# Kernel optimization log

Measured on AMD Instinct MI355X. Metric: run time of the kernel, lower is better.

## Reference

```python
import jax, jax.numpy as jnp
import numpy as np

N_NODES = 500_000
N_EDGES = 16_000_000


def setup_inputs() -> dict:
    key = jax.random.key(0)
    ks = jax.random.split(key, 8)
    x = jax.random.normal(ks[0], (N_NODES, 6), dtype=jnp.float32)
    edge_index = jax.random.randint(ks[1], (2, N_EDGES), 0, N_NODES, dtype=jnp.int64)
    conv_w = jax.random.normal(ks[2], (4, 6), dtype=jnp.float32) * 0.4
    conv_b = jax.random.normal(ks[3], (4,), dtype=jnp.float32) * 0.1
    fc1_w = jax.random.normal(ks[4], (64, 4), dtype=jnp.float32) * 0.5
    fc1_b = jax.random.normal(ks[5], (64,), dtype=jnp.float32) * 0.1
    fc3_w = jax.random.normal(ks[6], (10, 64), dtype=jnp.float32) * 0.125
    fc3_b = jax.random.normal(ks[7], (10,), dtype=jnp.float32) * 0.1
    return {"x": x, "edge_index": edge_index, "conv_w": conv_w, "conv_b": conv_b,
            "fc1_w": fc1_w, "fc1_b": fc1_b, "fc3_w": fc3_w, "fc3_b": fc3_b}


def reference(x, edge_index, conv_w, conv_b, fc1_w, fc1_b, fc3_w, fc3_b):
    n = x.shape[0]
    loop = jnp.arange(n, dtype=edge_index.dtype)
    # PyG GCNConv default: add self-loops, symmetric normalization
    row = jnp.concatenate([edge_index[0], loop])  # source
    col = jnp.concatenate([edge_index[1], loop])  # target (aggregation index)
    deg = jax.ops.segment_sum(jnp.ones_like(col, dtype=x.dtype), col, num_segments=n)
    dinv = jnp.where(deg > 0, deg ** -0.5, 0.0).astype(x.dtype)
    norm = dinv[row] * dinv[col]                  # [E+N]
    h = x @ conv_w.T                              # [N, 4]
    msg = h[row] * norm[:, None]                  # gather + scale
    agg = jax.ops.segment_sum(msg, col, num_segments=n) + conv_b  # scatter-add
    t = jnp.tanh(agg)
    # F.dropout treated as identity (deterministic eval reference)
    g = jnp.mean(t, axis=0, keepdims=True)        # global_mean_pool, batch=None -> [1, 4]
    hdn = jax.nn.relu(g @ fc1_w.T + fc1_b)
    out = hdn @ fc3_w.T + fc3_b                   # [1, output_size]
    return out
```

## Files before the change

### kernel.cpp

```cpp
#include <hip/hip_runtime.h>
#include <hip/hip_fp16.h>
#include <math.h>


constexpr int NP = 1024;
constexpr int SHIFT = 10;
constexpr unsigned MASK = 1023;
constexpr int NPART_MAX = 512;
constexpr int EPB = 8192;
constexpr int BINB = 512;
constexpr int BT = 512;

struct alignas(8) Half4 { __half2 a, b; };


__global__ __launch_bounds__(BINB) void k_bin(const int* __restrict__ row,
                                              const int* __restrict__ col, int E,
                                              int P, int cap, int* __restrict__ cursor,
                                              unsigned* __restrict__ binned) {
    __shared__ unsigned lbuf[EPB];
    __shared__ int lcount[NPART_MAX];
    __shared__ int lbase[NPART_MAX];
    __shared__ int gbase[NPART_MAX];
    __shared__ int lpos[NPART_MAX];
    __shared__ int sc[NPART_MAX];

    int t = threadIdx.x;
    int start = blockIdx.x * EPB;
    int end = min(start + EPB, E);
    bool full = (end - start) == EPB;

    lcount[t] = 0; lpos[t] = 0;
    __syncthreads();

    if (full) {
        const int4* c4 = (const int4*)(col + start);
#pragma unroll
        for (int i = 0; i < EPB / 4 / BINB; ++i) {
            int4 c = c4[t + i * BINB];
            atomicAdd(&lcount[c.x >> SHIFT], 1);
            atomicAdd(&lcount[c.y >> SHIFT], 1);
            atomicAdd(&lcount[c.z >> SHIFT], 1);
            atomicAdd(&lcount[c.w >> SHIFT], 1);
        }
    } else {
        for (int e = start + t; e < end; e += BINB)
            atomicAdd(&lcount[col[e] >> SHIFT], 1);
    }
    __syncthreads();

    sc[t] = lcount[t];
    __syncthreads();
    for (int off = 1; off < NPART_MAX; off <<= 1) {
        int v = (t >= off) ? sc[t - off] : 0;
        __syncthreads();
        sc[t] += v;
        __syncthreads();
    }
    lbase[t] = sc[t] - lcount[t];
    if (t < P) {
        int c = lcount[t];
        gbase[t] = (c > 0) ? atomicAdd(&cursor[t], c) : 0;
    }
    __syncthreads();

    if (full) {
        const int4* c4 = (const int4*)(col + start);
        const int4* r4 = (const int4*)(row + start);
#pragma unroll
        for (int i = 0; i < EPB / 4 / BINB; ++i) {
            int4 c = c4[t + i * BINB];
            int4 r = r4[t + i * BINB];
            int part, slot;
            part = c.x >> SHIFT; slot = atomicAdd(&lpos[part], 1);
            lbuf[lbase[part] + slot] = ((unsigned)r.x << SHIFT) | ((unsigned)c.x & MASK);
            part = c.y >> SHIFT; slot = atomicAdd(&lpos[part], 1);
            lbuf[lbase[part] + slot] = ((unsigned)r.y << SHIFT) | ((unsigned)c.y & MASK);
            part = c.z >> SHIFT; slot = atomicAdd(&lpos[part], 1);
            lbuf[lbase[part] + slot] = ((unsigned)r.z << SHIFT) | ((unsigned)c.z & MASK);
            part = c.w >> SHIFT; slot = atomicAdd(&lpos[part], 1);
            lbuf[lbase[part] + slot] = ((unsigned)r.w << SHIFT) | ((unsigned)c.w & MASK);
        }
    } else {
        for (int e = start + t; e < end; e += BINB) {
            int r = row[e], c = col[e];
            int part = c >> SHIFT;
            int slot = atomicAdd(&lpos[part], 1);
            lbuf[lbase[part] + slot] = ((unsigned)r << SHIFT) | ((unsigned)c & MASK);
        }
    }
    __syncthreads();

    int lane = t & 63;
    int wave = t >> 6;
    const int nwaves = BINB / 64;
    for (int part = wave; part < P; part += nwaves) {
        int cnt = lcount[part];
        if (cnt == 0) continue;
        int lb = lbase[part];
        int gb = gbase[part];
        unsigned* dst = binned + (size_t)part * cap;
        for (int j = lane; j < cnt; j += 64) {
            int slot = gb + j;
            if (slot < cap) dst[slot] = lbuf[lb + j];
        }
    }
}

__global__ __launch_bounds__(BT) void k_part_node(const unsigned* __restrict__ binned,
                                                  const int* __restrict__ cursor, int cap,
                                                  const float* __restrict__ x,
                                                  const float* __restrict__ conv_w, int n,
                                                  Half4* __restrict__ ph,
                                                  float* __restrict__ dinvg) {
    __shared__ int degs[NP];
    __shared__ float w[24];
    int part = blockIdx.x;
    int tid = threadIdx.x;
    if (tid < 24) w[tid] = conv_w[tid];
    for (int i = tid; i < NP; i += BT) degs[i] = 0;
    __syncthreads();
    int cnt = min(cursor[part], cap);
    const unsigned* bin = binned + (size_t)part * cap;
    const uint4* bin4 = (const uint4*)bin;
    int cnt4 = cnt >> 2;
    for (int i = tid; i < cnt4; i += BT) {
        uint4 v = bin4[i];
        atomicAdd(&degs[v.x & MASK], 1);
        atomicAdd(&degs[v.y & MASK], 1);
        atomicAdd(&degs[v.z & MASK], 1);
        atomicAdd(&degs[v.w & MASK], 1);
    }
    for (int e = (cnt4 << 2) + tid; e < cnt; e += BT)
        atomicAdd(&degs[bin[e] & MASK], 1);
    __syncthreads();
    int base = part * NP;
    for (int i = tid; i < NP; i += BT) {
        int node = base + i;
        if (node >= n) continue;
        float dinv = rsqrtf((float)(degs[i] + 1));
        const float* xr = x + (size_t)node * 6;
        float2 a = *(const float2*)xr;
        float2 b = *(const float2*)(xr + 2);
        float2 cc = *(const float2*)(xr + 4);
        float xv[6] = {a.x, a.y, b.x, b.y, cc.x, cc.y};
        float h0 = 0.f, h1 = 0.f, h2 = 0.f, h3 = 0.f;
#pragma unroll
        for (int j = 0; j < 6; ++j) {
            h0 += xv[j] * w[j];
            h1 += xv[j] * w[6 + j];
            h2 += xv[j] * w[12 + j];
            h3 += xv[j] * w[18 + j];
        }
        Half4 o;
        o.a = __floats2half2_rn(h0 * dinv, h1 * dinv);
        o.b = __floats2half2_rn(h2 * dinv, h3 * dinv);
        ph[node] = o;
        dinvg[node] = dinv;
    }
}

__global__ __launch_bounds__(BT) void k_acc(const unsigned* __restrict__ binned,
                                            const int* __restrict__ cursor, int cap,
                                            const Half4* __restrict__ ph,
                                            const float* __restrict__ dinvg,
                                            const float* __restrict__ conv_b, int n,
                                            float* __restrict__ gsum) {
    __shared__ float S[NP * 5];
    __shared__ float4 red[BT / 64];
    int part = blockIdx.x;
    int tid = threadIdx.x;
    for (int i = tid; i < NP * 5; i += BT) S[i] = 0.f;
    __syncthreads();
    int cnt = min(cursor[part], cap);
    const unsigned* bin = binned + (size_t)part * cap;
    const uint4* bin4 = (const uint4*)bin;
    int cnt4 = cnt >> 2;
    for (int i = tid; i < cnt4; i += BT) {
        uint4 v = bin4[i];
        Half4 h0 = ph[v.x >> SHIFT];
        Half4 h1 = ph[v.y >> SHIFT];
        Half4 h2 = ph[v.z >> SHIFT];
        Half4 h3 = ph[v.w >> SHIFT];
        float2 a, b; float* s;
        a = __half22float2(h0.a); b = __half22float2(h0.b); s = &S[(v.x & MASK) * 5];
        atomicAdd(s + 0, a.x); atomicAdd(s + 1, a.y); atomicAdd(s + 2, b.x); atomicAdd(s + 3, b.y);
        a = __half22float2(h1.a); b = __half22float2(h1.b); s = &S[(v.y & MASK) * 5];
        atomicAdd(s + 0, a.x); atomicAdd(s + 1, a.y); atomicAdd(s + 2, b.x); atomicAdd(s + 3, b.y);
        a = __half22float2(h2.a); b = __half22float2(h2.b); s = &S[(v.z & MASK) * 5];
        atomicAdd(s + 0, a.x); atomicAdd(s + 1, a.y); atomicAdd(s + 2, b.x); atomicAdd(s + 3, b.y);
        a = __half22float2(h3.a); b = __half22float2(h3.b); s = &S[(v.w & MASK) * 5];
        atomicAdd(s + 0, a.x); atomicAdd(s + 1, a.y); atomicAdd(s + 2, b.x); atomicAdd(s + 3, b.y);
    }
    for (int e = (cnt4 << 2) + tid; e < cnt; e += BT) {
        unsigned v = bin[e];
        Half4 h = ph[v >> SHIFT];
        float2 a = __half22float2(h.a), b = __half22float2(h.b);
        float* s = &S[(v & MASK) * 5];
        atomicAdd(s + 0, a.x); atomicAdd(s + 1, a.y); atomicAdd(s + 2, b.x); atomicAdd(s + 3, b.y);
    }
    __syncthreads();
    float b0 = conv_b[0], b1 = conv_b[1], b2 = conv_b[2], b3 = conv_b[3];
    float4 acc = {0.f, 0.f, 0.f, 0.f};
    int base = part * NP;
    for (int i = tid; i < NP; i += BT) {
        int node = base + i;
        if (node >= n) continue;
        float di = dinvg[node];
        Half4 hp = ph[node];
        float2 pa = __half22float2(hp.a), pb = __half22float2(hp.b);
        acc.x += tanhf(di * (S[i * 5 + 0] + pa.x) + b0);
        acc.y += tanhf(di * (S[i * 5 + 1] + pa.y) + b1);
        acc.z += tanhf(di * (S[i * 5 + 2] + pb.x) + b2);
        acc.w += tanhf(di * (S[i * 5 + 3] + pb.y) + b3);
    }
#pragma unroll
    for (int off = 32; off > 0; off >>= 1) {
        acc.x += __shfl_down(acc.x, off);
        acc.y += __shfl_down(acc.y, off);
        acc.z += __shfl_down(acc.z, off);
        acc.w += __shfl_down(acc.w, off);
    }
    int lane = tid & 63, wv = tid >> 6;
    if (lane == 0) red[wv] = acc;
    __syncthreads();
    if (tid == 0) {
        float4 tt = red[0];
        for (int k = 1; k < BT / 64; ++k) {
            tt.x += red[k].x; tt.y += red[k].y; tt.z += red[k].z; tt.w += red[k].w;
        }
        unsafeAtomicAdd(&gsum[0], tt.x);
        unsafeAtomicAdd(&gsum[1], tt.y);
        unsafeAtomicAdd(&gsum[2], tt.z);
        unsafeAtomicAdd(&gsum[3], tt.w);
    }
}

__global__ void k_head(const float* __restrict__ gsum,
                       const float* __restrict__ fc1w, const float* __restrict__ fc1b,
                       const float* __restrict__ fc3w, const float* __restrict__ fc3b,
                       float* __restrict__ out, int n) {
    __shared__ float hdn[64];
    int t = threadIdx.x;
    float g[4];
    float inv_n = 1.0f / (float)n;
#pragma unroll
    for (int j = 0; j < 4; ++j) g[j] = gsum[j] * inv_n;
    if (t < 64) {
        float a = fc1b[t];
#pragma unroll
        for (int j = 0; j < 4; ++j) a += g[j] * fc1w[t * 4 + j];
        hdn[t] = fmaxf(a, 0.f);
    }
    __syncthreads();
    if (t < 10) {
        float a = fc3b[t];
#pragma unroll
        for (int k = 0; k < 64; ++k) a += hdn[k] * fc3w[t * 64 + k];
        out[t] = a;
    }
}


__global__ void k_deg(const int* __restrict__ col, int n_edges, int* __restrict__ deg) {
    int t = blockIdx.x * blockDim.x + threadIdx.x;
    int base = t * 4;
    if (base + 4 <= n_edges) {
        int4 c = *(const int4*)(col + base);
        atomicAdd(&deg[c.x], 1); atomicAdd(&deg[c.y], 1);
        atomicAdd(&deg[c.z], 1); atomicAdd(&deg[c.w], 1);
    } else {
        for (int e = base; e < n_edges; ++e) atomicAdd(&deg[col[e]], 1);
    }
}

__global__ void k_node(const float* __restrict__ x, const float* __restrict__ conv_w,
                       const int* __restrict__ deg, float4* __restrict__ p, int n) {
    int i = blockIdx.x * blockDim.x + threadIdx.x;
    if (i >= n) return;
    const float* xr = x + (size_t)i * 6;
    float2 a = *(const float2*)xr;
    float2 b = *(const float2*)(xr + 2);
    float2 c = *(const float2*)(xr + 4);
    float xv[6] = {a.x, a.y, b.x, b.y, c.x, c.y};
    float dinv = rsqrtf((float)(deg[i] + 1));
    float h0 = 0.f, h1 = 0.f, h2 = 0.f, h3 = 0.f;
#pragma unroll
    for (int j = 0; j < 6; ++j) {
        h0 += xv[j] * conv_w[j];
        h1 += xv[j] * conv_w[6 + j];
        h2 += xv[j] * conv_w[12 + j];
        h3 += xv[j] * conv_w[18 + j];
    }
    float4 o; o.x = h0 * dinv; o.y = h1 * dinv; o.z = h2 * dinv; o.w = h3 * dinv;
    p[i] = o;
}

__global__ void k_scatter(const int* __restrict__ row, const int* __restrict__ col, int n_edges,
                          const float4* __restrict__ p, float* __restrict__ S) {
    int t = blockIdx.x * blockDim.x + threadIdx.x;
    int base = t * 2;
    if (base + 2 <= n_edges) {
        int2 r = *(const int2*)(row + base);
        int2 c = *(const int2*)(col + base);
        float4 p0 = p[r.x], p1 = p[r.y];
        float* s0 = S + 4 * c.x;
        unsafeAtomicAdd(s0 + 0, p0.x); unsafeAtomicAdd(s0 + 1, p0.y);
        unsafeAtomicAdd(s0 + 2, p0.z); unsafeAtomicAdd(s0 + 3, p0.w);
        float* s1 = S + 4 * c.y;
        unsafeAtomicAdd(s1 + 0, p1.x); unsafeAtomicAdd(s1 + 1, p1.y);
        unsafeAtomicAdd(s1 + 2, p1.z); unsafeAtomicAdd(s1 + 3, p1.w);
    } else {
        for (int e = base; e < n_edges; ++e) {
            int r = row[e], c = col[e];
            float4 pv = p[r];
            float* s = S + 4 * c;
            unsafeAtomicAdd(s + 0, pv.x); unsafeAtomicAdd(s + 1, pv.y);
            unsafeAtomicAdd(s + 2, pv.z); unsafeAtomicAdd(s + 3, pv.w);
        }
    }
}

__global__ void k_reduce(const float4* __restrict__ S4, const float4* __restrict__ p,
                         const int* __restrict__ deg, const float* __restrict__ conv_b,
                         int n, float* __restrict__ gsum) {
    int i = blockIdx.x * blockDim.x + threadIdx.x;
    float4 v = {0.f, 0.f, 0.f, 0.f};
    if (i < n) {
        float dinv = rsqrtf((float)(deg[i] + 1));
        float4 s = S4[i];
        float4 pp = p[i];
        v.x = tanhf(dinv * (s.x + pp.x) + conv_b[0]);
        v.y = tanhf(dinv * (s.y + pp.y) + conv_b[1]);
        v.z = tanhf(dinv * (s.z + pp.z) + conv_b[2]);
        v.w = tanhf(dinv * (s.w + pp.w) + conv_b[3]);
    }
#pragma unroll
    for (int off = 32; off > 0; off >>= 1) {
        v.x += __shfl_down(v.x, off);
        v.y += __shfl_down(v.y, off);
        v.z += __shfl_down(v.z, off);
        v.w += __shfl_down(v.w, off);
    }
    __shared__ float4 lds[4];
    int lane = threadIdx.x & 63, w = threadIdx.x >> 6;
    if (lane == 0) lds[w] = v;
    __syncthreads();
    if (threadIdx.x == 0) {
        float4 tt = lds[0];
        for (int k = 1; k < 4; ++k) {
            tt.x += lds[k].x; tt.y += lds[k].y; tt.z += lds[k].z; tt.w += lds[k].w;
        }
        unsafeAtomicAdd(&gsum[0], tt.x); unsafeAtomicAdd(&gsum[1], tt.y);
        unsafeAtomicAdd(&gsum[2], tt.z); unsafeAtomicAdd(&gsum[3], tt.w);
    }
}


extern "C" void kernel_launch(void* const* d_in, const int* in_sizes, int n_in,
                              void* d_out, int out_size, void* d_ws, size_t ws_size,
                              hipStream_t stream) {
    const float* x      = (const float*)d_in[0];
    const int*   ei     = (const int*)d_in[1];
    const float* conv_w = (const float*)d_in[2];
    const float* conv_b = (const float*)d_in[3];
    const float* fc1w   = (const float*)d_in[4];
    const float* fc1b   = (const float*)d_in[5];
    const float* fc3w   = (const float*)d_in[6];
    const float* fc3b   = (const float*)d_in[7];

    int n = in_sizes[0] / 6;
    int E = in_sizes[1] / 2;
    const int* row = ei;
    const int* col = ei + E;

    int P = (n + NP - 1) / NP;
    int avg = (E + P - 1) / P;
    int cap = ((avg + avg / 8 + 2048) + 15) & ~15;

    size_t off = 0;
    size_t cursor_off = off;          off += (size_t)P * sizeof(int);
    off = (off + 15) & ~(size_t)15;
    size_t gsum_off = off;            off += 4 * sizeof(float);
    size_t zero_end = off;
    off = (off + 15) & ~(size_t)15;
    size_t dinv_off = off;            off += (size_t)n * sizeof(float);
    off = (off + 15) & ~(size_t)15;
    size_t ph_off = off;              off += (size_t)n * sizeof(Half4);
    off = (off + 15) & ~(size_t)15;
    size_t bin_off = off;             off += (size_t)P * cap * sizeof(unsigned);
    size_t need = off;

    char* ws = (char*)d_ws;
    bool use_bin = (ws_size >= need) && (P <= NPART_MAX) && (n < (1 << 22));

    if (use_bin) {
        int* cursor = (int*)(ws + cursor_off);
        float* gsum = (float*)(ws + gsum_off);
        float* dinvg = (float*)(ws + dinv_off);
        Half4* ph = (Half4*)(ws + ph_off);
        unsigned* binned = (unsigned*)(ws + bin_off);

        hipMemsetAsync(d_ws, 0, zero_end, stream);
        int bin_blocks = (E + EPB - 1) / EPB;
        k_bin<<<bin_blocks, BINB, 0, stream>>>(row, col, E, P, cap, cursor, binned);
        k_part_node<<<P, BT, 0, stream>>>(binned, cursor, cap, x, conv_w, n, ph, dinvg);
        k_acc<<<P, BT, 0, stream>>>(binned, cursor, cap, ph, dinvg, conv_b, n, gsum);
        k_head<<<1, 64, 0, stream>>>(gsum, fc1w, fc1b, fc3w, fc3b, (float*)d_out, n);
    } else {
        size_t o = 0;
        int* deg = (int*)(ws + o);      o += (size_t)n * sizeof(int);
        o = (o + 15) & ~(size_t)15;
        float* S = (float*)(ws + o);    o += (size_t)n * 4 * sizeof(float);
        float* gsum = (float*)(ws + o);
        size_t zend = o + 4 * sizeof(float);
        o = (zend + 15) & ~(size_t)15;
        float4* p = (float4*)(ws + o);

        hipMemsetAsync(d_ws, 0, zend, stream);
        int t1 = (E + 3) / 4;
        k_deg<<<(t1 + 255) / 256, 256, 0, stream>>>(col, E, deg);
        k_node<<<(n + 255) / 256, 256, 0, stream>>>(x, conv_w, deg, p, n);
        int t3 = (E + 1) / 2;
        k_scatter<<<(t3 + 255) / 256, 256, 0, stream>>>(row, col, E, p, S);
        k_reduce<<<(n + 255) / 256, 256, 0, stream>>>((const float4*)S, p, deg, conv_b, n, gsum);
        k_head<<<1, 64, 0, stream>>>(gsum, fc1w, fc1b, fc3w, fc3b, (float*)d_out, n);
    }
}
```

Measured before the change: 624.5 us.

## Split per-partition accumulation across sub-blocks and move tanh reduction to separate kernel

The accumulation kernel now runs SUB blocks per partition. Each block accumulates its share of the binned edges in shared memory and writes a partial sum array to global memory. A new kernel adds up the partials for each node, applies tanh and reduces the result into the global sum. The change also unrolls the edge loop by two, switches to unsafeAtomicAdd on shared memory, and shrinks the bin capacity slack. The aim is more parallelism: P is about 489 blocks on a large GPU, so this doubles it. The cost is an extra kernel launch, extra global traffic for the partials, and a higher risk of bin overflow with the smaller capacity.

```diff
diff --git a/kernel.cpp b/kernel.cpp
--- a/kernel.cpp
+++ b/kernel.cpp
@@ -160,15 +160,23 @@
     }
 }
 
-__global__ __launch_bounds__(BT) void k_acc(const unsigned* __restrict__ binned,
-                                            const int* __restrict__ cursor, int cap,
-                                            const Half4* __restrict__ ph,
-                                            const float* __restrict__ dinvg,
-                                            const float* __restrict__ conv_b, int n,
-                                            float* __restrict__ gsum) {
+__device__ __forceinline__ void acc_edge(float* __restrict__ S, unsigned v,
+                                         const Half4& h) {
+    float2 a = __half22float2(h.a), b = __half22float2(h.b);
+    float* s = &S[(v & MASK) * 5];
+    unsafeAtomicAdd(s + 0, a.x);
+    unsafeAtomicAdd(s + 1, a.y);
+    unsafeAtomicAdd(s + 2, b.x);
+    unsafeAtomicAdd(s + 3, b.y);
+}
+
+__global__ __launch_bounds__(BT) void k_acc2(const unsigned* __restrict__ binned,
+                                             const int* __restrict__ cursor, int cap,
+                                             const Half4* __restrict__ ph, int SUB,
+                                             float4* __restrict__ Spart) {
     __shared__ float S[NP * 5];
-    __shared__ float4 red[BT / 64];
-    int part = blockIdx.x;
+    int part = blockIdx.x / SUB;
+    int sub = blockIdx.x - part * SUB;
     int tid = threadIdx.x;
     for (int i = tid; i < NP * 5; i += BT) S[i] = 0.f;
     __syncthreads();
@@ -176,43 +184,72 @@
     const unsigned* bin = binned + (size_t)part * cap;
     const uint4* bin4 = (const uint4*)bin;
     int cnt4 = cnt >> 2;
-    for (int i = tid; i < cnt4; i += BT) {
+    int chunk4 = (cnt4 + SUB - 1) / SUB;
+    int s4 = sub * chunk4;
+    int e4 = min(cnt4, s4 + chunk4);
+
+    int i = s4 + tid;
+    for (; i + BT < e4; i += 2 * BT) {
+        uint4 v0 = bin4[i];
+        uint4 v1 = bin4[i + BT];
+        Half4 h0 = ph[v0.x >> SHIFT];
+        Half4 h1 = ph[v0.y >> SHIFT];
+        Half4 h2 = ph[v0.z >> SHIFT];
+        Half4 h3 = ph[v0.w >> SHIFT];
+        Half4 h4 = ph[v1.x >> SHIFT];
+        Half4 h5 = ph[v1.y >> SHIFT];
+        Half4 h6 = ph[v1.z >> SHIFT];
+        Half4 h7 = ph[v1.w >> SHIFT];
+        acc_edge(S, v0.x, h0); acc_edge(S, v0.y, h1);
+        acc_edge(S, v0.z, h2); acc_edge(S, v0.w, h3);
+        acc_edge(S, v1.x, h4); acc_edge(S, v1.y, h5);
+        acc_edge(S, v1.z, h6); acc_edge(S, v1.w, h7);
+    }
+    for (; i < e4; i += BT) {
         uint4 v = bin4[i];
         Half4 h0 = ph[v.x >> SHIFT];
         Half4 h1 = ph[v.y >> SHIFT];
         Half4 h2 = ph[v.z >> SHIFT];
         Half4 h3 = ph[v.w >> SHIFT];
-        float2 a, b; float* s;
-        a = __half22float2(h0.a); b = __half22float2(h0.b); s = &S[(v.x & MASK) * 5];
-        atomicAdd(s + 0, a.x); atomicAdd(s + 1, a.y); atomicAdd(s + 2, b.x); atomicAdd(s + 3, b.y);
-        a = __half22float2(h1.a); b = __half22float2(h1.b); s = &S[(v.y & MASK) * 5];
-        atomicAdd(s + 0, a.x); atomicAdd(s + 1, a.y); atomicAdd(s + 2, b.x); atomicAdd(s + 3, b.y);
-        a = __half22float2(h2.a); b = __half22float2(h2.b); s = &S[(v.z & MASK) * 5];
-        atomicAdd(s + 0, a.x); atomicAdd(s + 1, a.y); atomicAdd(s + 2, b.x); atomicAdd(s + 3, b.y);
-        a = __half22float2(h3.a); b = __half22float2(h3.b); s = &S[(v.w & MASK) * 5];
-        atomicAdd(s + 0, a.x); atomicAdd(s + 1, a.y); atomicAdd(s + 2, b.x); atomicAdd(s + 3, b.y);
-    }
-    for (int e = (cnt4 << 2) + tid; e < cnt; e += BT) {
-        unsigned v = bin[e];
-        Half4 h = ph[v >> SHIFT];
-        float2 a = __half22float2(h.a), b = __half22float2(h.b);
-        float* s = &S[(v & MASK) * 5];
-        atomicAdd(s + 0, a.x); atomicAdd(s + 1, a.y); atomicAdd(s + 2, b.x); atomicAdd(s + 3, b.y);
-    }
-    __syncthreads();
-    float b0 = conv_b[0], b1 = conv_b[1], b2 = conv_b[2], b3 = conv_b[3];
+        acc_edge(S, v.x, h0); acc_edge(S, v.y, h1);
+        acc_edge(S, v.z, h2); acc_edge(S, v.w, h3);
+    }
+    if (sub == SUB - 1) {
+        for (int e = (cnt4 << 2) + tid; e < cnt; e += BT)
+            acc_edge(S, bin[e], ph[bin[e] >> SHIFT]);
+    }
+    __syncthreads();
+    float4* dst = Spart + (size_t)blockIdx.x * NP;
+    for (int k = tid; k < NP; k += BT) {
+        float4 o;
+        o.x = S[k * 5 + 0]; o.y = S[k * 5 + 1];
+        o.z = S[k * 5 + 2]; o.w = S[k * 5 + 3];
+        dst[k] = o;
+    }
+}
+
+__global__ __launch_bounds__(BT) void k_tanh(const float4* __restrict__ Spart,
+                                             const Half4* __restrict__ ph,
+                                             const float* __restrict__ dinvg,
+                                             const float* __restrict__ conv_b,
+                                             int n, int SUB, float* __restrict__ gsum) {
+    int node = blockIdx.x * BT + threadIdx.x;
     float4 acc = {0.f, 0.f, 0.f, 0.f};
-    int base = part * NP;
-    for (int i = tid; i < NP; i += BT) {
-        int node = base + i;
-        if (node >= n) continue;
+    if (node < n) {
+        int part = node >> SHIFT;
+        int local = node & MASK;
+        float4 s = {0.f, 0.f, 0.f, 0.f};
+        for (int sub = 0; sub < SUB; ++sub) {
+            float4 t = Spart[((size_t)(part * SUB + sub)) * NP + local];
+            s.x += t.x; s.y += t.y; s.z += t.z; s.w += t.w;
+        }
         float di = dinvg[node];
         Half4 hp = ph[node];
         float2 pa = __half22float2(hp.a), pb = __half22float2(hp.b);
-        acc.x += tanhf(di * (S[i * 5 + 0] + pa.x) + b0);
-        acc.y += tanhf(di * (S[i * 5 + 1] + pa.y) + b1);
-        acc.z += tanhf(di * (S[i * 5 + 2] + pb.x) + b2);
-        acc.w += tanhf(di * (S[i * 5 + 3] + pb.y) + b3);
+        acc.x = tanhf(di * (s.x + pa.x) + conv_b[0]);
+        acc.y = tanhf(di * (s.y + pa.y) + conv_b[1]);
+        acc.z = tanhf(di * (s.z + pb.x) + conv_b[2]);
+        acc.w = tanhf(di * (s.w + pb.y) + conv_b[3]);
     }
 #pragma unroll
     for (int off = 32; off > 0; off >>= 1) {
@@ -221,10 +258,11 @@
         acc.z += __shfl_down(acc.z, off);
         acc.w += __shfl_down(acc.w, off);
     }
-    int lane = tid & 63, wv = tid >> 6;
+    __shared__ float4 red[BT / 64];
+    int lane = threadIdx.x & 63, wv = threadIdx.x >> 6;
     if (lane == 0) red[wv] = acc;
     __syncthreads();
-    if (tid == 0) {
+    if (threadIdx.x == 0) {
         float4 tt = red[0];
         for (int k = 1; k < BT / 64; ++k) {
             tt.x += red[k].x; tt.y += red[k].y; tt.z += red[k].z; tt.w += red[k].w;
@@ -376,7 +414,7 @@
 
     int P = (n + NP - 1) / NP;
     int avg = (E + P - 1) / P;
-    int cap = ((avg + avg / 8 + 2048) + 15) & ~15;
+    int cap = ((avg + avg / 32 + 256) + 15) & ~15;
 
     size_t off = 0;
     size_t cursor_off = off;          off += (size_t)P * sizeof(int);
@@ -389,23 +427,29 @@
     size_t ph_off = off;              off += (size_t)n * sizeof(Half4);
     off = (off + 15) & ~(size_t)15;
     size_t bin_off = off;             off += (size_t)P * cap * sizeof(unsigned);
-    size_t need = off;
+    off = (off + 255) & ~(size_t)255;
+    size_t spart_off = off;
+    size_t spart_bytes1 = (size_t)P * NP * sizeof(float4);
 
     char* ws = (char*)d_ws;
-    bool use_bin = (ws_size >= need) && (P <= NPART_MAX) && (n < (1 << 22));
-
-    if (use_bin) {
+    int SUB = 0;
+    if (ws_size >= spart_off + 2 * spart_bytes1 && P <= NPART_MAX && n < (1 << 22)) SUB = 2;
+    else if (ws_size >= spart_off + spart_bytes1 && P <= NPART_MAX && n < (1 << 22)) SUB = 1;
+
+    if (SUB > 0) {
         int* cursor = (int*)(ws + cursor_off);
         float* gsum = (float*)(ws + gsum_off);
         float* dinvg = (float*)(ws + dinv_off);
         Half4* ph = (Half4*)(ws + ph_off);
         unsigned* binned = (unsigned*)(ws + bin_off);
+        float4* Spart = (float4*)(ws + spart_off);
 
         hipMemsetAsync(d_ws, 0, zero_end, stream);
         int bin_blocks = (E + EPB - 1) / EPB;
         k_bin<<<bin_blocks, BINB, 0, stream>>>(row, col, E, P, cap, cursor, binned);
         k_part_node<<<P, BT, 0, stream>>>(binned, cursor, cap, x, conv_w, n, ph, dinvg);
-        k_acc<<<P, BT, 0, stream>>>(binned, cursor, cap, ph, dinvg, conv_b, n, gsum);
+        k_acc2<<<P * SUB, BT, 0, stream>>>(binned, cursor, cap, ph, SUB, Spart);
+        k_tanh<<<(n + BT - 1) / BT, BT, 0, stream>>>(Spart, ph, dinvg, conv_b, n, SUB, gsum);
         k_head<<<1, 64, 0, stream>>>(gsum, fc1w, fc1b, fc3w, fc3b, (float*)d_out, n);
     } else {
         size_t o = 0;
```

Result: slower. 679.8 us (+8.9%).
